# Performance work log

Hardware: AMD Instinct MI355X
Metric: run time of the kernel (lower is better)

## Reference

```python
import jax, jax.numpy as jnp
import numpy as np

B, T, C, E, K = 8, 2048, 1024, 8, 2
CAP = int(T / E * 1.25)  # expert capacity per batch row = 320


def setup_inputs() -> dict:
    key = jax.random.key(0)
    ks = jax.random.split(key, 6)
    s = lambda k, shape, fan: jax.random.normal(k, shape, jnp.float32) / np.sqrt(fan)
    return dict(
        x=jax.random.normal(ks[0], (B, T, C), jnp.float32),
        rw1=s(ks[1], (C, 4 * C), C), rb1=jnp.zeros((4 * C,), jnp.float32),
        rw2=s(ks[2], (4 * C, 4 * C), 4 * C), rb2=jnp.zeros((4 * C,), jnp.float32),
        rw3=s(ks[3], (4 * C, E), 4 * C), rb3=jnp.zeros((E,), jnp.float32),
        ew1=s(ks[4], (E, C, 4 * C), C), eb1=jnp.zeros((E, 4 * C), jnp.float32),
        ew2=s(ks[5], (E, 4 * C, C), 4 * C), eb2=jnp.zeros((E, C), jnp.float32),
    )


def reference(x, rw1, rb1, rw2, rb2, rw3, rb3, ew1, eb1, ew2, eb2):
    # Router (dropout is identity in eval): MLP -> softmax over experts
    h = jax.nn.relu(x @ rw1 + rb1)
    h = jax.nn.relu(h @ rw2 + rb2)
    probs = jax.nn.softmax(h @ rw3 + rb3, axis=-1)        # [B,T,E]
    topk_p, topk_e = jax.lax.top_k(probs, K)              # [B,T,K]

    b_ids = jnp.broadcast_to(jnp.arange(B)[:, None], (B, T))
    out = jnp.zeros_like(x)
    # Loop over small fixed number of experts (mirrors per-rank expert compute)
    for e in range(E):
        sel = (topk_e == e)                               # [B,T,K]
        mask = sel.any(-1)                                # token routed to expert e
        gate = (topk_p * sel).sum(-1)                     # unnormalized top-k prob
        pos = jnp.cumsum(mask, axis=1) - 1                # slot within capacity buffer
        keep = mask & (pos < CAP)                         # capacity truncation (drop overflow)
        pos_s = jnp.where(keep, pos, CAP)                 # CAP is out-of-range -> dropped
        # Dispatch: scatter kept tokens into [B, CAP, C] capacity-padded buffer
        buf = jnp.zeros((B, CAP, C), x.dtype).at[b_ids, pos_s].set(x, mode='drop')
        # Expert FFN on padded buffer
        y = jax.nn.relu(buf @ ew1[e] + eb1[e]) @ ew2[e] + eb2[e]
        # Combine: gather back to token positions, weight by gate
        g = y[b_ids, jnp.where(keep, pos, 0)]
        out = out + gate[..., None] * jnp.where(keep[..., None], g, jnp.zeros((), x.dtype))
    return out
```

## Files before the change

kernel.cpp:

```cpp
#include <hip/hip_runtime.h>
#include <stdint.h>

typedef _Float16 f16;
typedef _Float16 half8 __attribute__((ext_vector_type(8)));
typedef float f32x4 __attribute__((ext_vector_type(4)));

#define NF_MAX 2048
#define THETA  0.02f

__device__ __forceinline__ void gload16(const void* g, void* l) {
  __builtin_amdgcn_global_load_lds(
      (const __attribute__((address_space(1))) void*)g,
      (__attribute__((address_space(3))) void*)l, 16, 0, 0);
}

#define BAR() do { __builtin_amdgcn_s_barrier(); __builtin_amdgcn_sched_barrier(0); } while (0)
#define WAIT_VM8() do { asm volatile("s_waitcnt vmcnt(8)" ::: "memory"); __builtin_amdgcn_sched_barrier(0); } while (0)
#define WAIT_VM0() do { asm volatile("s_waitcnt vmcnt(0)" ::: "memory"); __builtin_amdgcn_sched_barrier(0); } while (0)

template<int EPI, bool SPLIT3>
__launch_bounds__(512, 2)
__global__ void gemm256(const f16* __restrict__ A0, const f16* __restrict__ A1,
                        const f16* __restrict__ B0, const f16* __restrict__ B1,
                        int N, int Kd, int lda, int ldb,
                        const int* __restrict__ rowsrcA, const f16* __restrict__ zeroPage,
                        const float* __restrict__ bias, int bias_stride, int rows_per_exp,
                        f16* __restrict__ oH, int ldo, float* __restrict__ oAcc,
                        const float* __restrict__ w3, float* __restrict__ oLog,
                        const int* __restrict__ nfp)
{
  __shared__ f16 lds[4 * 8192 * 2 + 512];
  f16* sA = lds;
  f16* sB = lds + 4 * 8192;
  f16* sDummy = lds + 8 * 8192;

  const int tid  = threadIdx.x;
  const int lane = tid & 63, w = tid >> 6;
  const int wm = w >> 2, wn = w & 3;

  const int gx  = gridDim.x;
  const int nwg = gx * gridDim.y;
  const int bid = blockIdx.y * gx + blockIdx.x;
  const int swz = (bid & 7) * (nwg >> 3) + (bid >> 3);
  const int by  = swz / gx, bx = swz - by * gx;
  const int m0  = by * 256, n0 = bx * 256;
  const int k0  = blockIdx.z * Kd;

  if (nfp) {
    int nf = *nfp; nf = nf < NF_MAX ? nf : NF_MAX;
    const int lim = (nf + 255) & ~255;
    if (m0 >= lim) return;
  }

  int e = 0;
  if (rows_per_exp > 0) e = m0 / rows_per_exp;
  const f16* Bh = B0 + (size_t)e * N * ldb;

  const int nk  = Kd >> 6;
  const int NIT = SPLIT3 ? 3 * nk : nk;

  const int sr  = lane & 15;
  const int sk8 = lane >> 4;

  size_t aoff[2], boff[2];
  bool az[2] = { false, false };
  #pragma unroll
  for (int jj = 0; jj < 2; ++jj) {
    const int arow = m0 + (jj * 8 + w) * 16 + sr;
    if (rowsrcA) {
      const int rs = rowsrcA[arow];
      az[jj] = (rs < 0);
      aoff[jj] = az[jj] ? 0 : (size_t)rs * lda;
    } else {
      aoff[jj] = (size_t)arow * lda;
    }
    boff[jj] = (size_t)(n0 + (jj * 8 + w) * 16 + sr) * ldb;
  }

  auto stageA = [&](const f16* base, int kk, int kc, f16* slotBase, bool valid) {
    #pragma unroll
    for (int jj = 0; jj < 2; ++jj) {
      const int mt = jj * 8 + w;
      f16* dst = valid ? (slotBase + mt * 512) : sDummy;
      const f16* src = az[jj] ? zeroPage
                              : base + aoff[jj] + (k0 + kk + kc * 32 + sk8 * 8);
      gload16(src, dst);
    }
  };
  auto stageB = [&](const f16* base, int kk, int kc, f16* slotBase, bool valid) {
    #pragma unroll
    for (int jj = 0; jj < 2; ++jj) {
      const int mt = jj * 8 + w;
      f16* dst = valid ? (slotBase + mt * 512) : sDummy;
      const f16* src = base + boff[jj] + (k0 + kk + kc * 32 + sk8 * 8);
      gload16(src, dst);
    }
  };

  struct It { const f16* Ab; const f16* Bb; int kk, kin, pass; };
  const f16* Ab0 = SPLIT3 ? A1 : A0;
  auto advance = [&](It& s) {
    if (s.kin + 1 < nk) { s.kin++; }
    else if (SPLIT3 && s.pass < 2) {
      s.kin = 0; s.pass++;
      s.Ab = (s.pass == 0) ? A1 : A0;
      s.Bb = (s.pass == 1) ? B1 : Bh;
    }
    s.kk = s.kin << 6;
  };
  It it1 = { Ab0, Bh, 64, 1, 0 };
  It it2 = { Ab0, Bh, 128, 2, 0 };

  stageA(Ab0, 0, 0, &sA[0], true);
  stageB(Bh,  0, 0, &sB[0], true);
  stageA(Ab0, 0, 1, &sA[8192], true);
  stageB(Bh,  0, 1, &sB[8192], true);
  stageA(it1.Ab, it1.kk, 0, &sA[2 * 8192], true);
  stageB(it1.Bb, it1.kk, 0, &sB[2 * 8192], true);
  WAIT_VM8();
  BAR();

  f32x4 acc[8][4] = {};
  const int aBase = wm * 8;
  const int bBase = wn * 4;

  auto mfma16 = [&](half8* af, half8* bf, int moff) {
    __builtin_amdgcn_s_setprio(1);
    #pragma unroll
    for (int mi = 0; mi < 4; ++mi)
      #pragma unroll
      for (int ni = 0; ni < 4; ++ni)
        acc[moff + mi][ni] = __builtin_amdgcn_mfma_f32_16x16x32_f16(
            af[mi], bf[ni], acc[moff + mi][ni], 0, 0, 0);
    __builtin_amdgcn_s_setprio(0);
  };
  auto rdA = [&](half8* dst, int slot, int mtb) {
    #pragma unroll
    for (int mi = 0; mi < 4; ++mi)
      dst[mi] = *(const half8*)&sA[slot * 8192 + (mtb + mi) * 512 + lane * 8];
  };
  auto rdB = [&](half8* dst, int slot) {
    #pragma unroll
    for (int ni = 0; ni < 4; ++ni)
      dst[ni] = *(const half8*)&sB[slot * 8192 + (bBase + ni) * 512 + lane * 8];
  };

  for (int t = 0; t < NIT; ++t) {
    const int sa0 = (2 * t) & 3, sa1 = sa0 ^ 1;
    const bool v1 = (t + 1 < NIT), v2 = (t + 2 < NIT);

    if (SPLIT3 && t == 2 * nk) {
      #pragma unroll
      for (int mi = 0; mi < 8; ++mi)
        #pragma unroll
        for (int ni = 0; ni < 4; ++ni)
          acc[mi][ni] = acc[mi][ni] * 2.44140625e-4f;
    }

    half8 aF[4], bF[4], aG[4];

    rdA(aF, sa0, aBase);
    rdB(bF, sa0);
    rdA(aG, sa0, aBase + 4);
    stageA(it1.Ab, it1.kk, 1, &sA[(sa0 ^ 3) * 8192], v1);
    BAR();
    mfma16(aF, bF, 0);
    BAR();

    stageB(it1.Bb, it1.kk, 1, &sB[(sa0 ^ 3) * 8192], v1);
    WAIT_VM8();
    BAR();
    mfma16(aG, bF, 4);
    BAR();

    rdA(aF, sa1, aBase);
    rdB(bF, sa1);
    rdA(aG, sa1, aBase + 4);
    stageA(it2.Ab, it2.kk, 0, &sA[sa0 * 8192], v2);
    BAR();
    mfma16(aF, bF, 0);
    BAR();

    stageB(it2.Bb, it2.kk, 0, &sB[sa0 * 8192], v2);
    WAIT_VM8();
    BAR();
    mfma16(aG, bF, 4);
    BAR();

    it1 = it2;
    advance(it2);
  }
  WAIT_VM0();

  float bv[4] = { 0.f, 0.f, 0.f, 0.f };
  if (bias) {
    #pragma unroll
    for (int ni = 0; ni < 4; ++ni) {
      const int col = n0 + wn * 64 + ni * 16 + (lane & 15);
      bv[ni] = bias[(size_t)e * bias_stride + col];
    }
  }

  if (EPI == 2) {
    f32x4 wlo[4], whi[4];
    #pragma unroll
    for (int ni = 0; ni < 4; ++ni) {
      const int col = n0 + wn * 64 + ni * 16 + (lane & 15);
      wlo[ni] = *(const f32x4*)(w3 + (size_t)col * 8);
      whi[ni] = *(const f32x4*)(w3 + (size_t)col * 8 + 4);
    }
    const int p = (n0 >> 8) * 4 + wn;
    #pragma unroll
    for (int mi = 0; mi < 8; ++mi) {
      #pragma unroll
      for (int r = 0; r < 4; ++r) {
        const int row = m0 + wm * 128 + mi * 16 + (lane >> 4) * 4 + r;
        f32x4 plo = {}, phi = {};
        #pragma unroll
        for (int ni = 0; ni < 4; ++ni) {
          const float v = fmaxf(acc[mi][ni][r] + bv[ni], 0.f);
          plo += v * wlo[ni];
          phi += v * whi[ni];
        }
        #pragma unroll
        for (int msk = 1; msk < 16; msk <<= 1) {
          #pragma unroll
          for (int q = 0; q < 4; ++q) {
            plo[q] += __shfl_xor(plo[q], msk);
            phi[q] += __shfl_xor(phi[q], msk);
          }
        }
        if ((lane & 15) == 0) {
          float* dst = oLog + ((size_t)p * ldo + row) * 8;
          *(f32x4*)dst = plo;
          *(f32x4*)(dst + 4) = phi;
        }
      }
    }
  } else {
    #pragma unroll
    for (int mi = 0; mi < 8; ++mi) {
      #pragma unroll
      for (int r = 0; r < 4; ++r) {
        const int row = m0 + wm * 128 + mi * 16 + (lane >> 4) * 4 + r;
        #pragma unroll
        for (int ni = 0; ni < 4; ++ni) {
          const int col = n0 + wn * 64 + ni * 16 + (lane & 15);
          if (EPI == 3) {
            atomicAdd(&oAcc[(size_t)row * ldo + col], acc[mi][ni][r]);
          } else {
            float v = acc[mi][ni][r] + bv[ni];
            if (EPI == 0) v = fmaxf(v, 0.f);
            oH[(size_t)row * ldo + col] = (f16)v;
          }
        }
      }
    }
  }
}

__global__ void split_x(const float* __restrict__ x, f16* __restrict__ hi,
                        f16* __restrict__ lo, int n)
{
  const int i = blockIdx.x * 256 + threadIdx.x;
  if (i * 8 >= n) return;
  const f32x4 a = ((const f32x4*)x)[2 * i];
  const f32x4 b = ((const f32x4*)x)[2 * i + 1];
  half8 h, l;
  #pragma unroll
  for (int j = 0; j < 4; ++j) {
    float v = a[j]; f16 hh = (f16)v;
    h[j] = hh; l[j] = (f16)((v - (float)hh) * 4096.0f);
    v = b[j]; hh = (f16)v;
    h[4 + j] = hh; l[4 + j] = (f16)((v - (float)hh) * 4096.0f);
  }
  ((half8*)hi)[i] = h;
  ((half8*)lo)[i] = l;
}

template<bool SPLIT>
__global__ void transpose_conv(const float* __restrict__ in, f16* __restrict__ oh,
                               f16* __restrict__ ol, int R, int Cc)
{
  __shared__ float tile[64][65];
  const size_t boff = (size_t)blockIdx.z * R * Cc;
  in += boff; oh += boff;
  if (SPLIT) ol += boff;
  const int c0 = blockIdx.x * 64, r0 = blockIdx.y * 64;
  #pragma unroll
  for (int i = 0; i < 16; ++i) {
    const int idx = i * 256 + threadIdx.x;
    const int r = idx >> 6, c = idx & 63;
    tile[r][c] = in[(size_t)(r0 + r) * Cc + (c0 + c)];
  }
  __syncthreads();
  #pragma unroll
  for (int i = 0; i < 16; ++i) {
    const int idx = i * 256 + threadIdx.x;
    const int ro = idx >> 6, co = idx & 63;
    const float v = tile[co][ro];
    const f16 h = (f16)v;
    const size_t o = (size_t)(c0 + ro) * R + (r0 + co);
    oh[o] = h;
    if (SPLIT) ol[o] = (f16)((v - (float)h) * 4096.0f);
  }
}

__global__ void topk_flag(const float* __restrict__ part, const float* __restrict__ b3,
                          int* __restrict__ eidx, float* __restrict__ gval,
                          int* __restrict__ flags, int* __restrict__ nfc)
{
  const int t = blockIdx.x * 256 + threadIdx.x;
  float l[8];
  #pragma unroll
  for (int e = 0; e < 8; ++e) l[e] = b3[e];
  for (int p = 0; p < 64; ++p) {
    const float* src = part + ((size_t)p * 16384 + t) * 8;
    const f32x4 a = *(const f32x4*)src;
    const f32x4 b = *(const f32x4*)(src + 4);
    #pragma unroll
    for (int q = 0; q < 4; ++q) { l[q] += a[q]; l[4 + q] += b[q]; }
  }
  float mx = l[0];
  #pragma unroll
  for (int e = 1; e < 8; ++e) mx = fmaxf(mx, l[e]);
  float ex[8], s = 0.f;
  #pragma unroll
  for (int e = 0; e < 8; ++e) { ex[e] = expf(l[e] - mx); s += ex[e]; }
  float p1 = -1.f, p2 = -1.f; int e1 = 0, e2 = 0;
  #pragma unroll
  for (int e = 0; e < 8; ++e) {
    const float pe = ex[e] / s;
    if (pe > p1)      { p2 = p1; e2 = e1; p1 = pe; e1 = e; }
    else if (pe > p2) { p2 = pe; e2 = e; }
  }
  eidx[t * 2] = e1; eidx[t * 2 + 1] = e2;
  gval[t * 2] = p1; gval[t * 2 + 1] = p2;
  float l1 = -1e30f, l2 = -1e30f, l3 = -1e30f;
  #pragma unroll
  for (int e = 0; e < 8; ++e) {
    const float le = l[e];
    if (le > l1)      { l3 = l2; l2 = l1; l1 = le; }
    else if (le > l2) { l3 = l2; l2 = le; }
    else if (le > l3) { l3 = le; }
  }
  if (l2 - l3 < THETA) {
    const int s0 = atomicAdd(nfc, 1);
    if (s0 < NF_MAX) flags[s0] = t;
  }
}

__global__ void post1(const float* __restrict__ h1r, const float* __restrict__ b1,
                      f16* __restrict__ hh, f16* __restrict__ hl,
                      const int* __restrict__ nfc)
{
  int nf = *nfc; nf = nf < NF_MAX ? nf : NF_MAX;
  const int lim = (nf + 255) & ~255;
  const int row = blockIdx.x;
  if (row >= lim) return;
  const int j = blockIdx.y * 2048 + threadIdx.x * 8;
  const float* src = h1r + (size_t)row * 4096 + j;
  const f32x4 a = *(const f32x4*)src;
  const f32x4 b = *(const f32x4*)(src + 4);
  half8 h, l;
  #pragma unroll
  for (int k = 0; k < 4; ++k) {
    float v = fmaxf(a[k] + b1[j + k], 0.f);
    f16 x = (f16)v; h[k] = x; l[k] = (f16)((v - (float)x) * 4096.0f);
    v = fmaxf(b[k] + b1[j + 4 + k], 0.f);
    x = (f16)v; h[4 + k] = x; l[4 + k] = (f16)((v - (float)x) * 4096.0f);
  }
  *(half8*)(hh + (size_t)row * 4096 + j) = h;
  *(half8*)(hl + (size_t)row * 4096 + j) = l;
}

__global__ void logits_exact(const float* __restrict__ h2r, const float* __restrict__ b2,
                             const float* __restrict__ w3, const float* __restrict__ b3,
                             const int* __restrict__ flags, const int* __restrict__ nfc,
                             int* __restrict__ eidx, float* __restrict__ gval)
{
  const int srow = blockIdx.x;
  int nf = *nfc; nf = nf < NF_MAX ? nf : NF_MAX;
  if (srow >= nf) return;
  const float* hrow = h2r + (size_t)srow * 4096;
  double p[8];
  #pragma unroll
  for (int e = 0; e < 8; ++e) p[e] = 0.0;
  for (int i = 0; i < 16; ++i) {
    const int k = i * 256 + threadIdx.x;
    const double h = (double)fmaxf(hrow[k] + b2[k], 0.f);
    const float* wp = w3 + (size_t)k * 8;
    #pragma unroll
    for (int e = 0; e < 8; ++e) p[e] += h * (double)wp[e];
  }
  #pragma unroll
  for (int e = 0; e < 8; ++e)
    for (int off = 32; off > 0; off >>= 1)
      p[e] += __shfl_down(p[e], off);
  __shared__ double sp[4][8];
  const int lane = threadIdx.x & 63, wv = threadIdx.x >> 6;
  if (lane == 0) {
    #pragma unroll
    for (int e = 0; e < 8; ++e) sp[wv][e] = p[e];
  }
  __syncthreads();
  if (threadIdx.x == 0) {
    float l[8];
    #pragma unroll
    for (int e = 0; e < 8; ++e)
      l[e] = (float)(sp[0][e] + sp[1][e] + sp[2][e] + sp[3][e] + (double)b3[e]);
    float mx = l[0];
    for (int e = 1; e < 8; ++e) mx = fmaxf(mx, l[e]);
    float ex[8], s = 0.f;
    for (int e = 0; e < 8; ++e) { ex[e] = expf(l[e] - mx); s += ex[e]; }
    float p1 = -1.f, p2 = -1.f; int e1 = 0, e2 = 0;
    for (int e = 0; e < 8; ++e) {
      const float pe = ex[e] / s;
      if (pe > p1)      { p2 = p1; e2 = e1; p1 = pe; e1 = e; }
      else if (pe > p2) { p2 = pe; e2 = e; }
    }
    const int tok = flags[srow];
    eidx[tok * 2] = e1; eidx[tok * 2 + 1] = e2;
    gval[tok * 2] = p1; gval[tok * 2 + 1] = p2;
  }
}

__global__ void route_scan(const int* __restrict__ eidx, const float* __restrict__ gval,
                           int* __restrict__ cnt, int* __restrict__ rowsrc,
                           int* __restrict__ tokslot)
{
  const int pair = blockIdx.x;
  const int e = pair >> 3, b = pair & 7;
  const int lane = threadIdx.x;
  int running = 0;
  for (int t0 = 0; t0 < 2048; t0 += 64) {
    const int t = t0 + lane;
    const int i2 = (b * 2048 + t) * 2;
    const int m0 = (eidx[i2] == e), m1 = (eidx[i2 + 1] == e);
    const int m = m0 | m1;
    const unsigned long long bal = __ballot(m);
    const int pos = running + __popcll(bal & ((1ull << lane) - 1ull));
    if (m && pos < 320) {
      const int slot = pair * 320 + pos;
      rowsrc[slot] = b * 2048 + t;
      tokslot[(b * 2048 + t) * 2 + (m0 ? 0 : 1)] = slot;
    }
    running += __popcll(bal);
  }
  const int c = running < 320 ? running : 320;
  for (int s = c + lane; s < 320; s += 64) rowsrc[pair * 320 + s] = -1;
  if (lane == 0) cnt[pair] = c;
}

__global__ void combine(const float* __restrict__ ybF, const int* __restrict__ tokslot,
                        const float* __restrict__ gval, const float* __restrict__ eb2,
                        float* __restrict__ out)
{
  const int t = blockIdx.x;
  const int c = threadIdx.x * 8;
  const int s0 = tokslot[t * 2], s1 = tokslot[t * 2 + 1];
  const float g0 = gval[t * 2], g1 = gval[t * 2 + 1];
  f32x4 a0 = {}, a1 = {};
  if (s0 >= 0) {
    const float* y = ybF + (size_t)s0 * 1024 + c;
    const float* bb = eb2 + (size_t)(s0 / 2560) * 1024 + c;
    a0 += g0 * (*(const f32x4*)y + *(const f32x4*)bb);
    a1 += g0 * (*(const f32x4*)(y + 4) + *(const f32x4*)(bb + 4));
  }
  if (s1 >= 0) {
    const float* y = ybF + (size_t)s1 * 1024 + c;
    const float* bb = eb2 + (size_t)(s1 / 2560) * 1024 + c;
    a0 += g1 * (*(const f32x4*)y + *(const f32x4*)bb);
    a1 += g1 * (*(const f32x4*)(y + 4) + *(const f32x4*)(bb + 4));
  }
  float* dst = out + (size_t)t * 1024 + c;
  *(f32x4*)dst = a0;
  *(f32x4*)(dst + 4) = a1;
}

extern "C" void kernel_launch(void* const* d_in, const int* in_sizes, int n_in,
                              void* d_out, int out_size, void* d_ws, size_t ws_size,
                              hipStream_t stream)
{
  (void)in_sizes; (void)n_in; (void)out_size;
  const float* x   = (const float*)d_in[0];
  const float* rw1 = (const float*)d_in[1];
  const float* rb1 = (const float*)d_in[2];
  const float* rw2 = (const float*)d_in[3];
  const float* rb2 = (const float*)d_in[4];
  const float* rw3 = (const float*)d_in[5];
  const float* rb3 = (const float*)d_in[6];
  const float* ew1 = (const float*)d_in[7];
  const float* eb1 = (const float*)d_in[8];
  const float* ew2 = (const float*)d_in[9];
  const float* eb2 = (const float*)d_in[10];

  constexpr size_t MB = 1024ull * 1024ull;
  constexpr size_t KB = 1024ull;
  char* ws = (char*)d_ws;
  if (ws_size < 401 * MB) return;

  f16*   h1f  = (f16*)(ws);
  f16*   ew1t = (f16*)(ws);
  f16*   ew2t = (f16*)(ws + 64 * MB);
  f16*   xhi  = (f16*)(ws + 128 * MB);
  char*  S    = ws + 160 * MB;
  int*   eidx   = (int*)(S);
  float* gval   = (float*)(S + 128 * KB);
  int*   cnt    = (int*)(S + 256 * KB);
  int*   nfc    = (int*)(S + 260 * KB);
  int*   flags  = (int*)(S + 264 * KB);
  int*   tokslot= (int*)(S + 272 * KB);
  int*   rowsrc = (int*)(S + 400 * KB);
  f16*   zeros  = (f16*)(S + 480 * KB);
  f16*   xlo    = (f16*)(ws + 161 * MB);
  f16*   rw1thi = (f16*)(ws + 193 * MB);
  f16*   rw1tlo = (f16*)(ws + 201 * MB);
  f16*   rw2thi = (f16*)(ws + 209 * MB);
  f16*   rw2tlo = (f16*)(ws + 241 * MB);
  float* part   = (float*)(ws + 273 * MB);
  float* h1r    = (float*)(ws + 305 * MB);
  float* h2r    = (float*)(ws + 337 * MB);
  f16*   h1rh   = (f16*)(ws + 369 * MB);
  f16*   h1rl   = (f16*)(ws + 385 * MB);
  f16*   h_e    = (f16*)(ws + 161 * MB);
  float* ybF    = (float*)(ws + 321 * MB);

  hipMemsetAsync(nfc, 0, 4, stream);
  hipMemsetAsync(tokslot, 0xFF, 128 * KB, stream);
  hipMemsetAsync(zeros, 0, 16 * KB, stream);
  hipMemsetAsync(h1r, 0, 64 * MB, stream);

  split_x<<<8192, 256, 0, stream>>>(x, xhi, xlo, 16384 * 1024);
  transpose_conv<true ><<<dim3(64, 16, 1), 256, 0, stream>>>(rw1, rw1thi, rw1tlo, 1024, 4096);
  transpose_conv<true ><<<dim3(64, 64, 1), 256, 0, stream>>>(rw2, rw2thi, rw2tlo, 4096, 4096);

  gemm256<0, false><<<dim3(16, 64), 512, 0, stream>>>(
      xhi, nullptr, rw1thi, nullptr, 4096, 1024, 1024, 1024,
      nullptr, nullptr, rb1, 0, 0,
      h1f, 4096, nullptr, nullptr, nullptr, nullptr);
  gemm256<2, false><<<dim3(16, 64), 512, 0, stream>>>(
      h1f, nullptr, rw2thi, nullptr, 4096, 4096, 4096, 4096,
      nullptr, nullptr, rb2, 0, 0,
      nullptr, 16384, nullptr, rw3, part, nullptr);
  topk_flag<<<64, 256, 0, stream>>>(part, rb3, eidx, gval, flags, nfc);

  gemm256<3, true><<<dim3(16, 8, 2), 512, 0, stream>>>(
      xhi, xlo, rw1thi, rw1tlo, 4096, 512, 1024, 1024,
      flags, zeros, nullptr, 0, 0,
      nullptr, 4096, h1r, nullptr, nullptr, nfc);
  post1<<<dim3(2048, 2), 256, 0, stream>>>(h1r, rb1, h1rh, h1rl, nfc);
  gemm256<3, true><<<dim3(16, 8, 4), 512, 0, stream>>>(
      h1rh, h1rl, rw2thi, rw2tlo, 4096, 1024, 4096, 4096,
      nullptr, nullptr, nullptr, 0, 0,
      nullptr, 4096, h2r, nullptr, nullptr, nfc);
  logits_exact<<<NF_MAX, 256, 0, stream>>>(h2r, rb2, rw3, rb3, flags, nfc,
                                           eidx, gval);

  route_scan<<<64, 64, 0, stream>>>(eidx, gval, cnt, rowsrc, tokslot);

  transpose_conv<false><<<dim3(64, 16, 8), 256, 0, stream>>>(ew1, ew1t, nullptr, 1024, 4096);
  transpose_conv<false><<<dim3(16, 64, 8), 256, 0, stream>>>(ew2, ew2t, nullptr, 4096, 1024);
  hipMemsetAsync(ybF, 0, 80 * MB, stream);

  gemm256<0, false><<<dim3(16, 80), 512, 0, stream>>>(
      xhi, nullptr, ew1t, nullptr, 4096, 1024, 1024, 1024,
      rowsrc, zeros, eb1, 4096, 2560,
      h_e, 4096, nullptr, nullptr, nullptr, nullptr);
  gemm256<3, false><<<dim3(4, 80, 4), 512, 0, stream>>>(
      h_e, nullptr, ew2t, nullptr, 1024, 1024, 4096, 4096,
      nullptr, nullptr, nullptr, 0, 2560,
      nullptr, 1024, ybF, nullptr, nullptr, nullptr);

  combine<<<16384, 128, 0, stream>>>(ybF, tokslot, gval, eb2, (float*)d_out);
}
```

Before: 1.894 ms.

## Merge MFMA phases per K-step and drop split-K for expert down-projection

The GEMM main loop now reads all eight A fragments before issuing both global stages, with one wait and barrier pair around a single 32-MFMA block instead of two 16-MFMA halves separated by extra barriers. The second expert GEMM switches from 4-way split-K with fp32 atomic accumulation into a zeroed buffer to a single full-K launch whose epilogue adds the bias and writes fp16 output. This removes the 80 MB memset and the atomic traffic, and combine reads half-width data without a separate bias add. In exchange the down-projection grid has a quarter of the blocks, lowering parallelism, the A fragments raise register pressure, and storing the expert output in fp16 loses precision.

```diff
diff --git a/kernel.cpp b/kernel.cpp
--- a/kernel.cpp
+++ b/kernel.cpp
@@ -124,14 +124,14 @@
   const int aBase = wm * 8;
   const int bBase = wn * 4;
 
-  auto mfma16 = [&](half8* af, half8* bf, int moff) {
+  auto mfma32 = [&](half8* a8, half8* bf) {
     __builtin_amdgcn_s_setprio(1);
     #pragma unroll
-    for (int mi = 0; mi < 4; ++mi)
+    for (int mi = 0; mi < 8; ++mi)
       #pragma unroll
       for (int ni = 0; ni < 4; ++ni)
-        acc[moff + mi][ni] = __builtin_amdgcn_mfma_f32_16x16x32_f16(
-            af[mi], bf[ni], acc[moff + mi][ni], 0, 0, 0);
+        acc[mi][ni] = __builtin_amdgcn_mfma_f32_16x16x32_f16(
+            a8[mi], bf[ni], acc[mi][ni], 0, 0, 0);
     __builtin_amdgcn_s_setprio(0);
   };
   auto rdA = [&](half8* dst, int slot, int mtb) {
@@ -157,34 +157,26 @@
           acc[mi][ni] = acc[mi][ni] * 2.44140625e-4f;
     }
 
-    half8 aF[4], bF[4], aG[4];
-
-    rdA(aF, sa0, aBase);
+    half8 a8[8], bF[4];
+
+    rdA(&a8[0], sa0, aBase);
+    rdA(&a8[4], sa0, aBase + 4);
     rdB(bF, sa0);
-    rdA(aG, sa0, aBase + 4);
     stageA(it1.Ab, it1.kk, 1, &sA[(sa0 ^ 3) * 8192], v1);
-    BAR();
-    mfma16(aF, bF, 0);
-    BAR();
-
     stageB(it1.Bb, it1.kk, 1, &sB[(sa0 ^ 3) * 8192], v1);
     WAIT_VM8();
     BAR();
-    mfma16(aG, bF, 4);
+    mfma32(a8, bF);
     BAR();
 
-    rdA(aF, sa1, aBase);
+    rdA(&a8[0], sa1, aBase);
+    rdA(&a8[4], sa1, aBase + 4);
     rdB(bF, sa1);
-    rdA(aG, sa1, aBase + 4);
     stageA(it2.Ab, it2.kk, 0, &sA[sa0 * 8192], v2);
-    BAR();
-    mfma16(aF, bF, 0);
-    BAR();
-
     stageB(it2.Bb, it2.kk, 0, &sB[sa0 * 8192], v2);
     WAIT_VM8();
     BAR();
-    mfma16(aG, bF, 4);
+    mfma32(a8, bF);
     BAR();
 
     it1 = it2;
@@ -452,30 +444,27 @@
   if (lane == 0) cnt[pair] = c;
 }
 
-__global__ void combine(const float* __restrict__ ybF, const int* __restrict__ tokslot,
-                        const float* __restrict__ gval, const float* __restrict__ eb2,
-                        float* __restrict__ out)
+__global__ void combine(const f16* __restrict__ yb, const int* __restrict__ tokslot,
+                        const float* __restrict__ gval, float* __restrict__ out)
 {
   const int t = blockIdx.x;
-  const int c = threadIdx.x * 8;
   const int s0 = tokslot[t * 2], s1 = tokslot[t * 2 + 1];
   const float g0 = gval[t * 2], g1 = gval[t * 2 + 1];
-  f32x4 a0 = {}, a1 = {};
+  float a[8] = {};
   if (s0 >= 0) {
-    const float* y = ybF + (size_t)s0 * 1024 + c;
-    const float* bb = eb2 + (size_t)(s0 / 2560) * 1024 + c;
-    a0 += g0 * (*(const f32x4*)y + *(const f32x4*)bb);
-    a1 += g0 * (*(const f32x4*)(y + 4) + *(const f32x4*)(bb + 4));
+    const half8 y = ((const half8*)(yb + (size_t)s0 * 1024))[threadIdx.x];
+    #pragma unroll
+    for (int k = 0; k < 8; ++k) a[k] += g0 * (float)y[k];
   }
   if (s1 >= 0) {
-    const float* y = ybF + (size_t)s1 * 1024 + c;
-    const float* bb = eb2 + (size_t)(s1 / 2560) * 1024 + c;
-    a0 += g1 * (*(const f32x4*)y + *(const f32x4*)bb);
-    a1 += g1 * (*(const f32x4*)(y + 4) + *(const f32x4*)(bb + 4));
-  }
-  float* dst = out + (size_t)t * 1024 + c;
-  *(f32x4*)dst = a0;
-  *(f32x4*)(dst + 4) = a1;
+    const half8 y = ((const half8*)(yb + (size_t)s1 * 1024))[threadIdx.x];
+    #pragma unroll
+    for (int k = 0; k < 8; ++k) a[k] += g1 * (float)y[k];
+  }
+  float* dst = out + (size_t)t * 1024 + threadIdx.x * 8;
+  f32x4 lo = { a[0], a[1], a[2], a[3] }, hi = { a[4], a[5], a[6], a[7] };
+  *(f32x4*)dst = lo;
+  *(f32x4*)(dst + 4) = hi;
 }
 
 extern "C" void kernel_launch(void* const* d_in, const int* in_sizes, int n_in,
@@ -524,7 +513,7 @@
   f16*   h1rh   = (f16*)(ws + 369 * MB);
   f16*   h1rl   = (f16*)(ws + 385 * MB);
   f16*   h_e    = (f16*)(ws + 161 * MB);
-  float* ybF    = (float*)(ws + 321 * MB);
+  f16*   yb     = (f16*)(ws + 321 * MB);
 
   hipMemsetAsync(nfc, 0, 4, stream);
   hipMemsetAsync(tokslot, 0xFF, 128 * KB, stream);
@@ -561,16 +550,15 @@
 
   transpose_conv<false><<<dim3(64, 16, 8), 256, 0, stream>>>(ew1, ew1t, nullptr, 1024, 4096);
   transpose_conv<false><<<dim3(16, 64, 8), 256, 0, stream>>>(ew2, ew2t, nullptr, 4096, 1024);
-  hipMemsetAsync(ybF, 0, 80 * MB, stream);
 
   gemm256<0, false><<<dim3(16, 80), 512, 0, stream>>>(
       xhi, nullptr, ew1t, nullptr, 4096, 1024, 1024, 1024,
       rowsrc, zeros, eb1, 4096, 2560,
       h_e, 4096, nullptr, nullptr, nullptr, nullptr);
-  gemm256<3, false><<<dim3(4, 80, 4), 512, 0, stream>>>(
-      h_e, nullptr, ew2t, nullptr, 1024, 1024, 4096, 4096,
-      nullptr, nullptr, nullptr, 0, 2560,
-      nullptr, 1024, ybF, nullptr, nullptr, nullptr);
-
-  combine<<<16384, 128, 0, stream>>>(ybF, tokslot, gval, eb2, (float*)d_out);
-}
+  gemm256<1, false><<<dim3(4, 80), 512, 0, stream>>>(
+      h_e, nullptr, ew2t, nullptr, 1024, 4096, 4096, 4096,
+      nullptr, nullptr, eb2, 1024, 2560,
+      yb, 1024, nullptr, nullptr, nullptr, nullptr);
+
+  combine<<<16384, 128, 0, stream>>>(yb, tokslot, gval, (float*)d_out);
+}
```

Result: faster. 1.821 ms (-3.8%).
